# Kernel optimization log

Measured on AMD Instinct MI355X. Metric: run time of the kernel, lower is better.

## Reference

```python
import jax, jax.numpy as jnp
import numpy as np

IN_FEAT, H_FEAT, NUM_CLASSES = 7, 8, 2
N_NODES, N_EDGES, N_GRAPHS = 40000, 640000, 64
DIMS = [IN_FEAT, H_FEAT, H_FEAT * 2, H_FEAT * 4, H_FEAT * 8, H_FEAT * 16]  # 7,8,16,32,64,128


def setup_inputs() -> dict:
    key = jax.random.key(0)
    ks = jax.random.split(key, 20)
    inp = {
        "x": jax.random.normal(ks[0], (N_NODES, IN_FEAT), dtype=jnp.float32),
        "edge_index": jax.random.randint(ks[1], (2, N_EDGES), 0, N_NODES, dtype=jnp.int32),
        "edge_attr": jax.random.uniform(ks[2], (N_EDGES,), dtype=jnp.float32),
        "batch": jnp.sort(jax.random.randint(ks[3], (N_NODES,), 0, N_GRAPHS, dtype=jnp.int32)),
    }
    # GraphConv params: lin_rel (with bias) applied to aggregated messages,
    # lin_root (no bias) applied to x itself. Stored as [in, out]; y = x @ W.
    for i in range(5):
        fi, fo = DIMS[i], DIMS[i + 1]
        s = 1.0 / np.sqrt(fi)
        inp[f"w_rel{i+1}"] = jax.random.uniform(ks[4 + 3 * i], (fi, fo), minval=-s, maxval=s, dtype=jnp.float32)
        inp[f"b_rel{i+1}"] = jax.random.uniform(ks[5 + 3 * i], (fo,), minval=-s, maxval=s, dtype=jnp.float32)
        inp[f"w_root{i+1}"] = jax.random.uniform(ks[6 + 3 * i], (fi, fo), minval=-s, maxval=s, dtype=jnp.float32)
    s = 1.0 / np.sqrt(DIMS[-1])
    inp["w_lin"] = jax.random.uniform(ks[19], (DIMS[-1], NUM_CLASSES), minval=-s, maxval=s, dtype=jnp.float32)
    inp["b_lin"] = jax.random.uniform(jax.random.fold_in(key, 99), (NUM_CLASSES,), minval=-s, maxval=s, dtype=jnp.float32)
    return inp


def graph_conv(x, src, dst, ew, w_rel, b_rel, w_root):
    # message: edge_weight * x[src]; aggregate by sum at dst (PyG GraphConv, aggr='add')
    msg = x[src] * ew[:, None]                               # [E, Fin]
    agg = jax.ops.segment_sum(msg, dst, num_segments=N_NODES)  # [N, Fin]
    return agg @ w_rel + b_rel + x @ w_root                  # [N, Fout]


def reference(x, edge_index, edge_attr, batch,
              w_rel1, b_rel1, w_root1, w_rel2, b_rel2, w_root2,
              w_rel3, b_rel3, w_root3, w_rel4, b_rel4, w_root4,
              w_rel5, b_rel5, w_root5, w_lin, b_lin):
    src, dst = edge_index[0], edge_index[1]
    h = x
    params = [(w_rel1, b_rel1, w_root1), (w_rel2, b_rel2, w_root2),
              (w_rel3, b_rel3, w_root3), (w_rel4, b_rel4, w_root4),
              (w_rel5, b_rel5, w_root5)]
    for wr, br, wo in params:
        h = graph_conv(h, src, dst, edge_attr, wr, br, wo)
    pooled = jax.ops.segment_sum(h, batch, num_segments=N_GRAPHS)  # [G, 128]
    return pooled @ w_lin + b_lin                                  # [G, 2]
```

## Files before the change

### kernel.cpp

```cpp
#include <hip/hip_runtime.h>

#define N_NODES 40000
#define N_EDGES 640000
#define N_GRAPHS 64

typedef unsigned short u16;
typedef unsigned int u32;
typedef __attribute__((ext_vector_type(8))) short bf16x8;
typedef __attribute__((ext_vector_type(4))) float f32x4;

static inline int cdiv(long long a, int b) { return (int)((a + b - 1) / b); }

__device__ __forceinline__ u16 f2bf(float f) {
    u32 u = __float_as_uint(f);
    u32 r = (u + 0x7fffu + ((u >> 16) & 1u)) >> 16;
    return (u16)r;
}
__device__ __forceinline__ u32 packpair(float a, float b) {
    return (u32)f2bf(a) | ((u32)f2bf(b) << 16);
}
__device__ __forceinline__ void unpack8(uint4 q, float* o) {
    o[0] = __uint_as_float(q.x << 16); o[1] = __uint_as_float(q.x & 0xffff0000u);
    o[2] = __uint_as_float(q.y << 16); o[3] = __uint_as_float(q.y & 0xffff0000u);
    o[4] = __uint_as_float(q.z << 16); o[5] = __uint_as_float(q.z & 0xffff0000u);
    o[6] = __uint_as_float(q.w << 16); o[7] = __uint_as_float(q.w & 0xffff0000u);
}
__device__ __forceinline__ void fma4(float4& a, float s, const float4& w) {
    a.x = fmaf(s, w.x, a.x);
    a.y = fmaf(s, w.y, a.y);
    a.z = fmaf(s, w.z, a.z);
    a.w = fmaf(s, w.w, a.w);
}

__global__ __launch_bounds__(256) void hist_kernel(const int* __restrict__ dst,
                                                   int* __restrict__ deg) {
    int e = blockIdx.x * 256 + threadIdx.x;
    if (e < N_EDGES) atomicAdd(&deg[dst[e]], 1);
}

__global__ __launch_bounds__(1024) void scan_part(const int* __restrict__ deg,
                                                  int* __restrict__ row_start,
                                                  int* __restrict__ bsum) {
    __shared__ int wtot[16], woff[16];
    int tid = threadIdx.x;
    int i = blockIdx.x * 1024 + tid;
    int v = (i < N_NODES) ? deg[i] : 0;
    int lane = tid & 63, wid = tid >> 6;
    int inc = v;
    #pragma unroll
    for (int off = 1; off < 64; off <<= 1) {
        int y = __shfl_up(inc, off, 64);
        if (lane >= off) inc += y;
    }
    if (lane == 63) wtot[wid] = inc;
    __syncthreads();
    if (tid < 16) {
        int b = wtot[tid];
        #pragma unroll
        for (int off = 1; off < 16; off <<= 1) {
            int y = __shfl_up(b, off, 16);
            if ((tid & 15) >= off) b += y;
        }
        woff[tid] = b - wtot[tid];
        if (tid == 15) bsum[blockIdx.x] = b;
    }
    __syncthreads();
    if (i <= N_NODES) row_start[i] = woff[wid] + inc - v;
}

__global__ __launch_bounds__(1024) void scan_add(int* __restrict__ row_start,
                                                 const int* __restrict__ bsum,
                                                 int* __restrict__ cursor) {
    __shared__ int sbase;
    int tid = threadIdx.x;
    if (tid < 64) {
        int b = (tid < blockIdx.x) ? bsum[tid] : 0;
        #pragma unroll
        for (int off = 32; off; off >>= 1) b += __shfl_xor(b, off, 64);
        if (tid == 0) sbase = b;
    }
    __syncthreads();
    int i = blockIdx.x * 1024 + tid;
    if (i <= N_NODES) {
        int v = row_start[i] + sbase;
        row_start[i] = v;
        if (i < N_NODES) cursor[i] = v;
    }
}

__global__ __launch_bounds__(256) void scatter_kernel(const int* __restrict__ src,
                                                      const int* __restrict__ dst,
                                                      const float* __restrict__ ew,
                                                      int* __restrict__ cursor,
                                                      int2* __restrict__ csr_pair) {
    int e = blockIdx.x * 256 + threadIdx.x;
    if (e >= N_EDGES) return;
    int pos = atomicAdd(&cursor[dst[e]], 1);
    int2 q;
    q.x = src[e];
    q.y = __float_as_int(ew[e]);
    csr_pair[pos] = q;
}

__device__ __forceinline__ void pack_one(int idx, int K, int FOUT,
                                         const float* __restrict__ wrel,
                                         const float* __restrict__ wroot,
                                         u16* __restrict__ out) {
    int j = idx & 7;
    int lane = (idx >> 3) & 63;
    int ksnt = idx >> 9;
    int KS = K >> 5;
    int nt = ksnt / KS, ks = ksnt - nt * KS;
    int k = ks * 32 + (lane >> 4) * 8 + j;
    int col = nt * 16 + (lane & 15);
    float v = (k < K / 2) ? wrel[k * FOUT + col] : wroot[(k - K / 2) * FOUT + col];
    out[idx] = f2bf(v);
}

__global__ __launch_bounds__(256) void pack_weights(const float* __restrict__ wr3, const float* __restrict__ wo3,
                                                    const float* __restrict__ wr4, const float* __restrict__ wo4,
                                                    const float* __restrict__ wr5, const float* __restrict__ wo5,
                                                    u16* __restrict__ p3, u16* __restrict__ p4, u16* __restrict__ p5) {
    int tid = blockIdx.x * 256 + threadIdx.x;
    if (tid < 1024)        pack_one(tid,         32,  32,  wr3, wo3, p3);
    else if (tid < 5120)   pack_one(tid - 1024,  64,  64,  wr4, wo4, p4);
    else if (tid < 21504)  pack_one(tid - 5120, 128, 128,  wr5, wo5, p5);
}

template<int SLOG>
__global__ __launch_bounds__(256) void gather1(const float* __restrict__ x,
                                               const int* __restrict__ rs,
                                               const int2* __restrict__ pair,
                                               float* __restrict__ agg) {
    const int S = 1 << SLOG;
    long long tid = (long long)blockIdx.x * 256 + threadIdx.x;
    int n = (int)(tid >> (3 + SLOG));
    if (n >= N_NODES) return;
    int sub = (int)(tid & ((8 << SLOG) - 1));
    int f = sub & 7;
    int half = sub >> 3;
    int beg = rs[n], end = rs[n + 1];
    float acc = 0.f;
    int p = beg + half;
    int s = 0; float w = 0.f;
    if (p < end) { int2 q = pair[p]; s = q.x; w = __int_as_float(q.y); }
    while (p < end) {
        float v = (f < 7) ? x[(long long)s * 7 + f] : 0.f;
        float wc = w;
        int pn = p + S;
        if (pn < end) { int2 q = pair[pn]; s = q.x; w = __int_as_float(q.y); }
        acc = fmaf(wc, v, acc);
        p = pn;
    }
    #pragma unroll
    for (int d = 8; d < (8 << SLOG); d <<= 1) acc += __shfl_xor(acc, d, 64);
    if (half == 0 && f < 7) agg[(long long)n * 7 + f] = acc;
}

template<int LOGF, int SLOG, int IN_STRIDE, int IN_OFF, int OUT_STRIDE, int OUT_OFF>
__global__ __launch_bounds__(256) void gather_bf16(const u16* __restrict__ hbuf,
                                                   const int* __restrict__ rs,
                                                   const int2* __restrict__ pair,
                                                   u16* __restrict__ obuf) {
    const int S = 1 << SLOG;
    long long tid = (long long)blockIdx.x * 256 + threadIdx.x;
    int n = (int)(tid >> (LOGF + SLOG));
    if (n >= N_NODES) return;
    int sub = (int)(tid & ((1 << (LOGF + SLOG)) - 1));
    int c = sub & ((1 << LOGF) - 1);
    int half = sub >> LOGF;
    const u16* base = hbuf + IN_OFF + c * 8;
    int beg = rs[n], end = rs[n + 1];
    float acc[8] = {0.f, 0.f, 0.f, 0.f, 0.f, 0.f, 0.f, 0.f};
    int p = beg + half;
    int s = 0; float w = 0.f;
    if (p < end) { int2 q = pair[p]; s = q.x; w = __int_as_float(q.y); }
    while (p < end) {
        uint4 rq = *(const uint4*)(base + (long long)s * IN_STRIDE);
        float wc = w;
        int pn = p + S;
        if (pn < end) { int2 q = pair[pn]; s = q.x; w = __int_as_float(q.y); }
        float tv[8];
        unpack8(rq, tv);
        #pragma unroll
        for (int j = 0; j < 8; ++j) acc[j] = fmaf(wc, tv[j], acc[j]);
        p = pn;
    }
    #pragma unroll
    for (int d = (1 << LOGF); d < (1 << (LOGF + SLOG)); d <<= 1) {
        #pragma unroll
        for (int j = 0; j < 8; ++j) acc[j] += __shfl_xor(acc[j], d, 64);
    }
    if (half == 0) {
        uint4 o;
        o.x = packpair(acc[0], acc[1]); o.y = packpair(acc[2], acc[3]);
        o.z = packpair(acc[4], acc[5]); o.w = packpair(acc[6], acc[7]);
        *(uint4*)(obuf + (long long)n * OUT_STRIDE + OUT_OFF + c * 8) = o;
    }
}

__global__ __launch_bounds__(256) void node1(const float* __restrict__ agg,
                                             const float* __restrict__ x,
                                             const float* __restrict__ wr,
                                             const float* __restrict__ br,
                                             const float* __restrict__ wo,
                                             u16* __restrict__ obuf) {
    __shared__ float swr[56], swo[56], sb[8];
    if (threadIdx.x < 56) { swr[threadIdx.x] = wr[threadIdx.x]; swo[threadIdx.x] = wo[threadIdx.x]; }
    if (threadIdx.x < 8) sb[threadIdx.x] = br[threadIdx.x];
    __syncthreads();
    int n = blockIdx.x * 256 + threadIdx.x;
    if (n >= N_NODES) return;
    float a[7], h[7];
    #pragma unroll
    for (int i = 0; i < 7; ++i) {
        a[i] = agg[(long long)n * 7 + i];
        h[i] = x[(long long)n * 7 + i];
    }
    float o[8];
    #pragma unroll
    for (int j = 0; j < 8; ++j) {
        float s = sb[j];
        #pragma unroll
        for (int i = 0; i < 7; ++i) s = fmaf(a[i], swr[i * 8 + j], fmaf(h[i], swo[i * 8 + j], s));
        o[j] = s;
    }
    uint4 q;
    q.x = packpair(o[0], o[1]); q.y = packpair(o[2], o[3]);
    q.z = packpair(o[4], o[5]); q.w = packpair(o[6], o[7]);
    *(uint4*)(obuf + (long long)n * 16 + 8) = q;
}

template<int K, int FOUT, int FO_TILE, int NT, int OUT_STRIDE, int OUT_OFF>
__global__ __launch_bounds__(256) void node_mm(const u16* __restrict__ abuf,
                                               const float* __restrict__ w_rel,
                                               const float* __restrict__ b_rel,
                                               const float* __restrict__ w_root,
                                               u16* __restrict__ obuf) {
    constexpr int FG = FO_TILE / 4;
    constexpr int SLOTS = 256 / FG;
    constexpr int BN = SLOTS * NT;
    __shared__ float sw[K][FO_TILE];
    for (int i = threadIdx.x; i < K * FO_TILE; i += 256) {
        int k = i / FO_TILE, j = i % FO_TILE;
        sw[k][j] = (k < K / 2) ? w_rel[k * FOUT + j]
                               : w_root[(k - K / 2) * FOUT + j];
    }
    __syncthreads();
    int fg = threadIdx.x % FG;
    int slot = threadIdx.x / FG;
    int n0 = blockIdx.x * BN + slot * NT;
    float4 bias = *(const float4*)&b_rel[fg * 4];
    float4 acc[NT];
    #pragma unroll
    for (int t = 0; t < NT; ++t) acc[t] = bias;

    #pragma unroll
    for (int kc = 0; kc < K / 8; ++kc) {
        float4 wv[8];
        #pragma unroll
        for (int k = 0; k < 8; ++k) wv[k] = *(const float4*)&sw[kc * 8 + k][fg * 4];
        #pragma unroll
        for (int t = 0; t < NT; ++t) {
            int n = n0 + t;
            if (n < N_NODES) {
                uint4 q = *(const uint4*)(abuf + (long long)n * K + kc * 8);
                float av[8];
                unpack8(q, av);
                #pragma unroll
                for (int k = 0; k < 8; ++k) fma4(acc[t], av[k], wv[k]);
            }
        }
    }
    #pragma unroll
    for (int t = 0; t < NT; ++t) {
        int n = n0 + t;
        if (n < N_NODES) {
            uint2 o;
            o.x = packpair(acc[t].x, acc[t].y);
            o.y = packpair(acc[t].z, acc[t].w);
            *(uint2*)(obuf + (long long)n * OUT_STRIDE + OUT_OFF + fg * 4) = o;
        }
    }
}

template<int K, int FOUT, int OUT_STRIDE, int OUT_OFF, bool POOL>
__global__ __launch_bounds__(64) void node_mfma(const u16* __restrict__ abuf,
                                                const u16* __restrict__ bpack,
                                                const float* __restrict__ b_rel,
                                                u16* __restrict__ obuf,
                                                const int* __restrict__ batch,
                                                float* __restrict__ pooled) {
    constexpr int NT = FOUT / 16;
    constexpr int KS = K / 32;
    int lane = threadIdx.x;
    int tile = blockIdx.x;
    int col = lane & 15;
    int node_a = tile * 16 + col;
    int kgrp = (lane >> 4) * 8;

    f32x4 acc[NT];
    #pragma unroll
    for (int nt = 0; nt < NT; ++nt) {
        float bv = b_rel[nt * 16 + col];
        acc[nt] = (f32x4){bv, bv, bv, bv};
    }

    const u16* arow = abuf + (long long)node_a * K + kgrp;
    #pragma unroll
    for (int ks = 0; ks < KS; ++ks) {
        bf16x8 af = *(const bf16x8*)(arow + ks * 32);
        #pragma unroll
        for (int nt = 0; nt < NT; ++nt) {
            bf16x8 bf = *(const bf16x8*)(bpack + (((nt * KS + ks) << 6) + lane) * 8);
            acc[nt] = __builtin_amdgcn_mfma_f32_16x16x32_bf16(af, bf, acc[nt], 0, 0, 0);
        }
    }

    int row0 = tile * 16 + (lane >> 4) * 4;
    if constexpr (!POOL) {
        #pragma unroll
        for (int nt = 0; nt < NT; ++nt)
            #pragma unroll
            for (int r = 0; r < 4; ++r)
                obuf[(long long)(row0 + r) * OUT_STRIDE + OUT_OFF + nt * 16 + col] =
                    f2bf(acc[nt][r]);
    } else {
        int b_first = batch[tile * 16];
        int b_last = batch[tile * 16 + 15];
        if (b_first == b_last) {
            #pragma unroll
            for (int nt = 0; nt < NT; ++nt) {
                float s = acc[nt][0] + acc[nt][1] + acc[nt][2] + acc[nt][3];
                s += __shfl_xor(s, 16, 64);
                s += __shfl_xor(s, 32, 64);
                if (lane < 16) atomicAdd(&pooled[b_first * FOUT + nt * 16 + col], s);
            }
        } else {
            #pragma unroll
            for (int r = 0; r < 4; ++r) {
                int g = batch[row0 + r];
                #pragma unroll
                for (int nt = 0; nt < NT; ++nt)
                    atomicAdd(&pooled[g * FOUT + nt * 16 + col], acc[nt][r]);
            }
        }
    }
}

__global__ void final_kernel(const float* __restrict__ pooled,
                             const float* __restrict__ w_lin,
                             const float* __restrict__ b_lin,
                             float* __restrict__ out) {
    int tid = threadIdx.x;
    int g = tid >> 1;
    int c = tid & 1;
    float acc = b_lin[c];
    #pragma unroll 8
    for (int fi = 0; fi < 128; ++fi)
        acc += pooled[g * 128 + fi] * w_lin[fi * 2 + c];
    out[g * 2 + c] = acc;
}

extern "C" void kernel_launch(void* const* d_in, const int* in_sizes, int n_in,
                              void* d_out, int out_size, void* d_ws, size_t ws_size,
                              hipStream_t stream) {
    const float* x     = (const float*)d_in[0];
    const int*   ei    = (const int*)d_in[1];
    const float* ea    = (const float*)d_in[2];
    const int*   batch = (const int*)d_in[3];
    const int* src = ei;
    const int* dst = ei + N_EDGES;

    const float* w_rel[5], *b_rel[5], *w_root[5];
    for (int i = 0; i < 5; ++i) {
        w_rel[i]  = (const float*)d_in[4 + 3 * i];
        b_rel[i]  = (const float*)d_in[5 + 3 * i];
        w_root[i] = (const float*)d_in[6 + 3 * i];
    }
    const float* w_lin = (const float*)d_in[19];
    const float* b_lin = (const float*)d_in[20];
    float* out = (float*)d_out;

    float* agg1    = (float*)d_ws;
    u16*   buf2    = (u16*)(agg1 + 280000);
    u16*   buf3    = buf2 + 640000;
    u16*   buf4    = buf3 + 1280000;
    u16*   buf5    = buf4 + 2560000;
    float* pooled  = (float*)(buf5 + 5120000);
    u16*   p3      = (u16*)(pooled + N_GRAPHS * 128);
    u16*   p4      = p3 + 1024;
    u16*   p5      = p4 + 4096;
    int2*  csr_pair= (int2*)(p5 + 16384);
    int*   deg     = (int*)(csr_pair + N_EDGES);
    int*   rs      = deg + N_NODES;
    int*   cursor  = rs + N_NODES + 1;
    int*   bsum    = cursor + N_NODES;

    const int BLK = 256;
    const int EB = cdiv(N_EDGES, BLK);

    pack_weights<<<84, BLK, 0, stream>>>(w_rel[2], w_root[2], w_rel[3], w_root[3],
                                         w_rel[4], w_root[4], p3, p4, p5);
    hipMemsetAsync(deg, 0, (size_t)N_NODES * sizeof(int), stream);
    hist_kernel<<<EB, BLK, 0, stream>>>(dst, deg);
    scan_part<<<40, 1024, 0, stream>>>(deg, rs, bsum);
    scan_add<<<40, 1024, 0, stream>>>(rs, bsum, cursor);
    scatter_kernel<<<EB, BLK, 0, stream>>>(src, dst, ea, cursor, csr_pair);

    gather1<2><<<cdiv((long long)N_NODES * 32, BLK), BLK, 0, stream>>>(x, rs, csr_pair, agg1);
    node1<<<cdiv(N_NODES, 256), BLK, 0, stream>>>(agg1, x, w_rel[0], b_rel[0], w_root[0], buf2);

    gather_bf16<0, 3, 16, 8, 16, 0><<<cdiv((long long)N_NODES * 8, BLK), BLK, 0, stream>>>(
        buf2, rs, csr_pair, buf2);
    node_mm<16, 16, 16, 4, 32, 16><<<cdiv(N_NODES, 256), BLK, 0, stream>>>(
        buf2, w_rel[1], b_rel[1], w_root[1], buf3);

    gather_bf16<1, 3, 32, 16, 32, 0><<<cdiv((long long)N_NODES * 16, BLK), BLK, 0, stream>>>(
        buf3, rs, csr_pair, buf3);
    node_mfma<32, 32, 64, 32, false><<<2500, 64, 0, stream>>>(
        buf3, p3, b_rel[2], buf4, nullptr, nullptr);

    gather_bf16<2, 3, 64, 32, 64, 0><<<cdiv((long long)N_NODES * 32, BLK), BLK, 0, stream>>>(
        buf4, rs, csr_pair, buf4);
    node_mfma<64, 64, 128, 64, false><<<2500, 64, 0, stream>>>(
        buf4, p4, b_rel[3], buf5, nullptr, nullptr);

    gather_bf16<3, 3, 128, 64, 128, 0><<<cdiv((long long)N_NODES * 64, BLK), BLK, 0, stream>>>(
        buf5, rs, csr_pair, buf5);
    hipMemsetAsync(pooled, 0, (size_t)N_GRAPHS * 128 * sizeof(float), stream);
    node_mfma<128, 128, 0, 0, true><<<2500, 64, 0, stream>>>(
        buf5, p5, b_rel[4], nullptr, batch, pooled);

    final_kernel<<<1, 128, 0, stream>>>(pooled, w_lin, b_lin, out);
}
```

Baseline: 254.1 us.

## Fuse per-layer neighbor gather with MFMA node transform via LDS staging

Measured after the change: 275.7 us. 1.09x slower.

```diff
diff --git a/kernel.cpp b/kernel.cpp
--- a/kernel.cpp
+++ b/kernel.cpp
@@ -24,12 +24,6 @@
     o[2] = __uint_as_float(q.y << 16); o[3] = __uint_as_float(q.y & 0xffff0000u);
     o[4] = __uint_as_float(q.z << 16); o[5] = __uint_as_float(q.z & 0xffff0000u);
     o[6] = __uint_as_float(q.w << 16); o[7] = __uint_as_float(q.w & 0xffff0000u);
-}
-__device__ __forceinline__ void fma4(float4& a, float s, const float4& w) {
-    a.x = fmaf(s, w.x, a.x);
-    a.y = fmaf(s, w.y, a.y);
-    a.z = fmaf(s, w.z, a.z);
-    a.w = fmaf(s, w.w, a.w);
 }
 
 __global__ __launch_bounds__(256) void hist_kernel(const int* __restrict__ dst,
@@ -102,59 +96,48 @@
     csr_pair[pos] = q;
 }
 
-__device__ __forceinline__ void pack_one(int idx, int K, int FOUT,
+__device__ __forceinline__ void pack_one(int idx, int KS, int Kreal, int FOUT,
                                          const float* __restrict__ wrel,
                                          const float* __restrict__ wroot,
                                          u16* __restrict__ out) {
     int j = idx & 7;
     int lane = (idx >> 3) & 63;
-    int ksnt = idx >> 9;
-    int KS = K >> 5;
-    int nt = ksnt / KS, ks = ksnt - nt * KS;
+    int rest = idx >> 9;
+    int nt = rest / KS, ks = rest - nt * KS;
     int k = ks * 32 + (lane >> 4) * 8 + j;
     int col = nt * 16 + (lane & 15);
-    float v = (k < K / 2) ? wrel[k * FOUT + col] : wroot[(k - K / 2) * FOUT + col];
+    float v = 0.f;
+    if (k < Kreal / 2) v = wrel[k * FOUT + col];
+    else if (k < Kreal) v = wroot[(k - Kreal / 2) * FOUT + col];
     out[idx] = f2bf(v);
 }
 
-__global__ __launch_bounds__(256) void pack_weights(const float* __restrict__ wr3, const float* __restrict__ wo3,
-                                                    const float* __restrict__ wr4, const float* __restrict__ wo4,
-                                                    const float* __restrict__ wr5, const float* __restrict__ wo5,
-                                                    u16* __restrict__ p3, u16* __restrict__ p4, u16* __restrict__ p5) {
+__global__ __launch_bounds__(256) void pack_weights(
+        const float* __restrict__ wr2, const float* __restrict__ wo2,
+        const float* __restrict__ wr3, const float* __restrict__ wo3,
+        const float* __restrict__ wr4, const float* __restrict__ wo4,
+        const float* __restrict__ wr5, const float* __restrict__ wo5,
+        u16* __restrict__ p2, u16* __restrict__ p3,
+        u16* __restrict__ p4, u16* __restrict__ p5) {
     int tid = blockIdx.x * 256 + threadIdx.x;
-    if (tid < 1024)        pack_one(tid,         32,  32,  wr3, wo3, p3);
-    else if (tid < 5120)   pack_one(tid - 1024,  64,  64,  wr4, wo4, p4);
-    else if (tid < 21504)  pack_one(tid - 5120, 128, 128,  wr5, wo5, p5);
-}
-
-template<int SLOG>
-__global__ __launch_bounds__(256) void gather1(const float* __restrict__ x,
-                                               const int* __restrict__ rs,
-                                               const int2* __restrict__ pair,
-                                               float* __restrict__ agg) {
-    const int S = 1 << SLOG;
-    long long tid = (long long)blockIdx.x * 256 + threadIdx.x;
-    int n = (int)(tid >> (3 + SLOG));
+    if (tid < 512)         pack_one(tid,         1,  16,  16,  wr2, wo2, p2);
+    else if (tid < 1536)   pack_one(tid - 512,   1,  32,  32,  wr3, wo3, p3);
+    else if (tid < 5632)   pack_one(tid - 1536,  2,  64,  64,  wr4, wo4, p4);
+    else if (tid < 22016)  pack_one(tid - 5632,  4, 128, 128,  wr5, wo5, p5);
+}
+
+__global__ __launch_bounds__(256) void convert_x(const float* __restrict__ x,
+                                                 u16* __restrict__ xbf) {
+    int n = blockIdx.x * 256 + threadIdx.x;
     if (n >= N_NODES) return;
-    int sub = (int)(tid & ((8 << SLOG) - 1));
-    int f = sub & 7;
-    int half = sub >> 3;
-    int beg = rs[n], end = rs[n + 1];
-    float acc = 0.f;
-    int p = beg + half;
-    int s = 0; float w = 0.f;
-    if (p < end) { int2 q = pair[p]; s = q.x; w = __int_as_float(q.y); }
-    while (p < end) {
-        float v = (f < 7) ? x[(long long)s * 7 + f] : 0.f;
-        float wc = w;
-        int pn = p + S;
-        if (pn < end) { int2 q = pair[pn]; s = q.x; w = __int_as_float(q.y); }
-        acc = fmaf(wc, v, acc);
-        p = pn;
-    }
-    #pragma unroll
-    for (int d = 8; d < (8 << SLOG); d <<= 1) acc += __shfl_xor(acc, d, 64);
-    if (half == 0 && f < 7) agg[(long long)n * 7 + f] = acc;
+    float v[8];
+    #pragma unroll
+    for (int i = 0; i < 7; ++i) v[i] = x[n * 7 + i];
+    v[7] = 0.f;
+    uint4 q;
+    q.x = packpair(v[0], v[1]); q.y = packpair(v[2], v[3]);
+    q.z = packpair(v[4], v[5]); q.w = packpair(v[6], v[7]);
+    *(uint4*)(xbf + (long long)n * 8) = q;
 }
 
 template<int LOGF, int SLOG, int IN_STRIDE, int IN_OFF, int OUT_STRIDE, int OUT_OFF>
@@ -199,24 +182,23 @@
     }
 }
 
-__global__ __launch_bounds__(256) void node1(const float* __restrict__ agg,
-                                             const float* __restrict__ x,
-                                             const float* __restrict__ wr,
-                                             const float* __restrict__ br,
-                                             const float* __restrict__ wo,
-                                             u16* __restrict__ obuf) {
+__global__ __launch_bounds__(256) void node1b(const u16* __restrict__ agg1,
+                                              const u16* __restrict__ xbf,
+                                              const float* __restrict__ wr,
+                                              const float* __restrict__ br,
+                                              const float* __restrict__ wo,
+                                              u16* __restrict__ h2) {
     __shared__ float swr[56], swo[56], sb[8];
     if (threadIdx.x < 56) { swr[threadIdx.x] = wr[threadIdx.x]; swo[threadIdx.x] = wo[threadIdx.x]; }
     if (threadIdx.x < 8) sb[threadIdx.x] = br[threadIdx.x];
     __syncthreads();
     int n = blockIdx.x * 256 + threadIdx.x;
     if (n >= N_NODES) return;
-    float a[7], h[7];
-    #pragma unroll
-    for (int i = 0; i < 7; ++i) {
-        a[i] = agg[(long long)n * 7 + i];
-        h[i] = x[(long long)n * 7 + i];
-    }
+    float a[8], h[8];
+    uint4 qa = *(const uint4*)(agg1 + (long long)n * 8);
+    uint4 qh = *(const uint4*)(xbf + (long long)n * 8);
+    unpack8(qa, a);
+    unpack8(qh, h);
     float o[8];
     #pragma unroll
     for (int j = 0; j < 8; ++j) {
@@ -228,121 +210,136 @@
     uint4 q;
     q.x = packpair(o[0], o[1]); q.y = packpair(o[2], o[3]);
     q.z = packpair(o[4], o[5]); q.w = packpair(o[6], o[7]);
-    *(uint4*)(obuf + (long long)n * 16 + 8) = q;
-}
-
-template<int K, int FOUT, int FO_TILE, int NT, int OUT_STRIDE, int OUT_OFF>
-__global__ __launch_bounds__(256) void node_mm(const u16* __restrict__ abuf,
-                                               const float* __restrict__ w_rel,
-                                               const float* __restrict__ b_rel,
-                                               const float* __restrict__ w_root,
-                                               u16* __restrict__ obuf) {
-    constexpr int FG = FO_TILE / 4;
-    constexpr int SLOTS = 256 / FG;
-    constexpr int BN = SLOTS * NT;
-    __shared__ float sw[K][FO_TILE];
-    for (int i = threadIdx.x; i < K * FO_TILE; i += 256) {
-        int k = i / FO_TILE, j = i % FO_TILE;
-        sw[k][j] = (k < K / 2) ? w_rel[k * FOUT + j]
-                               : w_root[(k - K / 2) * FOUT + j];
+    *(uint4*)(h2 + (long long)n * 8) = q;
+}
+
+template<int LOGC, int FOUT, bool POOL>
+__global__ __launch_bounds__(256) void fused_layer(const u16* __restrict__ hin,
+                                                   const int* __restrict__ rs,
+                                                   const int2* __restrict__ pair,
+                                                   const u16* __restrict__ bpack,
+                                                   const float* __restrict__ b_rel,
+                                                   u16* __restrict__ hout,
+                                                   const int* __restrict__ batch,
+                                                   float* __restrict__ pooled) {
+    constexpr int FIN = 8 << LOGC;
+    constexpr int KREAL = 2 * FIN;
+    constexpr int K = (KREAL < 32) ? 32 : KREAL;
+    constexpr int KS = K / 32;
+    constexpr int NT = FOUT / 16;
+    constexpr int NTW = (NT + 3) / 4;
+    constexpr int LDK = K + 8;
+    constexpr int CHUNKS = 1 << LOGC;
+    constexpr int SPLIT = 64 >> LOGC;
+
+    __shared__ u16 lds[16][LDK];
+
+    int tid = threadIdx.x;
+    int wave = tid >> 6;
+    int lane = tid & 63;
+    int node0 = blockIdx.x * 16;
+
+    if constexpr (KREAL < K) {
+        for (int i = tid; i < 16 * (K - KREAL); i += 256) {
+            int r = i / (K - KREAL), cc = i % (K - KREAL);
+            lds[r][KREAL + cc] = 0;
+        }
+    }
+    {
+        constexpr int CH = FIN / 8;
+        for (int i = tid; i < 16 * CH; i += 256) {
+            int r = i / CH, cc = i % CH;
+            uint4 v = *(const uint4*)(hin + (long long)(node0 + r) * FIN + cc * 8);
+            *(uint4*)&lds[r][FIN + cc * 8] = v;
+        }
+    }
+
+    int c = lane & (CHUNKS - 1);
+    int half = lane >> LOGC;
+    #pragma unroll
+    for (int rnd = 0; rnd < 4; ++rnd) {
+        int nl = rnd * 4 + wave;
+        int n = node0 + nl;
+        int beg = rs[n], end = rs[n + 1];
+        float acc[8] = {0.f, 0.f, 0.f, 0.f, 0.f, 0.f, 0.f, 0.f};
+        int p = beg + half;
+        int s = 0; float w = 0.f;
+        if (p < end) { int2 q = pair[p]; s = q.x; w = __int_as_float(q.y); }
+        while (p < end) {
+            uint4 rq = *(const uint4*)(hin + (long long)s * FIN + c * 8);
+            float wc = w;
+            int pn = p + SPLIT;
+            if (pn < end) { int2 q = pair[pn]; s = q.x; w = __int_as_float(q.y); }
+            float tv[8];
+            unpack8(rq, tv);
+            #pragma unroll
+            for (int j = 0; j < 8; ++j) acc[j] = fmaf(wc, tv[j], acc[j]);
+            p = pn;
+        }
+        #pragma unroll
+        for (int d = CHUNKS; d < 64; d <<= 1) {
+            #pragma unroll
+            for (int j = 0; j < 8; ++j) acc[j] += __shfl_xor(acc[j], d, 64);
+        }
+        if (half == 0) {
+            uint4 o;
+            o.x = packpair(acc[0], acc[1]); o.y = packpair(acc[2], acc[3]);
+            o.z = packpair(acc[4], acc[5]); o.w = packpair(acc[6], acc[7]);
+            *(uint4*)&lds[nl][c * 8] = o;
+        }
     }
     __syncthreads();
-    int fg = threadIdx.x % FG;
-    int slot = threadIdx.x / FG;
-    int n0 = blockIdx.x * BN + slot * NT;
-    float4 bias = *(const float4*)&b_rel[fg * 4];
-    float4 acc[NT];
-    #pragma unroll
-    for (int t = 0; t < NT; ++t) acc[t] = bias;
-
-    #pragma unroll
-    for (int kc = 0; kc < K / 8; ++kc) {
-        float4 wv[8];
-        #pragma unroll
-        for (int k = 0; k < 8; ++k) wv[k] = *(const float4*)&sw[kc * 8 + k][fg * 4];
-        #pragma unroll
-        for (int t = 0; t < NT; ++t) {
-            int n = n0 + t;
-            if (n < N_NODES) {
-                uint4 q = *(const uint4*)(abuf + (long long)n * K + kc * 8);
-                float av[8];
-                unpack8(q, av);
-                #pragma unroll
-                for (int k = 0; k < 8; ++k) fma4(acc[t], av[k], wv[k]);
-            }
-        }
-    }
-    #pragma unroll
-    for (int t = 0; t < NT; ++t) {
-        int n = n0 + t;
-        if (n < N_NODES) {
-            uint2 o;
-            o.x = packpair(acc[t].x, acc[t].y);
-            o.y = packpair(acc[t].z, acc[t].w);
-            *(uint2*)(obuf + (long long)n * OUT_STRIDE + OUT_OFF + fg * 4) = o;
-        }
-    }
-}
-
-template<int K, int FOUT, int OUT_STRIDE, int OUT_OFF, bool POOL>
-__global__ __launch_bounds__(64) void node_mfma(const u16* __restrict__ abuf,
-                                                const u16* __restrict__ bpack,
-                                                const float* __restrict__ b_rel,
-                                                u16* __restrict__ obuf,
-                                                const int* __restrict__ batch,
-                                                float* __restrict__ pooled) {
-    constexpr int NT = FOUT / 16;
-    constexpr int KS = K / 32;
-    int lane = threadIdx.x;
-    int tile = blockIdx.x;
-    int col = lane & 15;
-    int node_a = tile * 16 + col;
-    int kgrp = (lane >> 4) * 8;
-
-    f32x4 acc[NT];
-    #pragma unroll
-    for (int nt = 0; nt < NT; ++nt) {
-        float bv = b_rel[nt * 16 + col];
-        acc[nt] = (f32x4){bv, bv, bv, bv};
-    }
-
-    const u16* arow = abuf + (long long)node_a * K + kgrp;
+
+    int ntbase = wave * NTW;
+    if (ntbase >= NT) return;
+
+    int colc = lane & 15;
+    int kg = (lane >> 4) * 8;
+
+    f32x4 acc[NTW];
+    #pragma unroll
+    for (int t = 0; t < NTW; ++t) {
+        float bv = b_rel[(ntbase + t) * 16 + colc];
+        acc[t] = (f32x4){bv, bv, bv, bv};
+    }
+
     #pragma unroll
     for (int ks = 0; ks < KS; ++ks) {
-        bf16x8 af = *(const bf16x8*)(arow + ks * 32);
-        #pragma unroll
-        for (int nt = 0; nt < NT; ++nt) {
-            bf16x8 bf = *(const bf16x8*)(bpack + (((nt * KS + ks) << 6) + lane) * 8);
-            acc[nt] = __builtin_amdgcn_mfma_f32_16x16x32_bf16(af, bf, acc[nt], 0, 0, 0);
-        }
-    }
-
-    int row0 = tile * 16 + (lane >> 4) * 4;
+        bf16x8 af = *(const bf16x8*)&lds[colc][kg + ks * 32];
+        #pragma unroll
+        for (int t = 0; t < NTW; ++t) {
+            int ntg = ntbase + t;
+            bf16x8 bf = *(const bf16x8*)(bpack + (((ntg * KS + ks) << 6) + lane) * 8);
+            acc[t] = __builtin_amdgcn_mfma_f32_16x16x32_bf16(af, bf, acc[t], 0, 0, 0);
+        }
+    }
+
+    int row0 = (lane >> 4) * 4;
     if constexpr (!POOL) {
         #pragma unroll
-        for (int nt = 0; nt < NT; ++nt)
+        for (int t = 0; t < NTW; ++t)
             #pragma unroll
             for (int r = 0; r < 4; ++r)
-                obuf[(long long)(row0 + r) * OUT_STRIDE + OUT_OFF + nt * 16 + col] =
-                    f2bf(acc[nt][r]);
+                hout[(long long)(node0 + row0 + r) * FOUT + (ntbase + t) * 16 + colc] =
+                    f2bf(acc[t][r]);
     } else {
-        int b_first = batch[tile * 16];
-        int b_last = batch[tile * 16 + 15];
+        int b_first = batch[node0];
+        int b_last = batch[node0 + 15];
         if (b_first == b_last) {
             #pragma unroll
-            for (int nt = 0; nt < NT; ++nt) {
-                float s = acc[nt][0] + acc[nt][1] + acc[nt][2] + acc[nt][3];
-                s += __shfl_xor(s, 16, 64);
-                s += __shfl_xor(s, 32, 64);
-                if (lane < 16) atomicAdd(&pooled[b_first * FOUT + nt * 16 + col], s);
+            for (int t = 0; t < NTW; ++t) {
+                float s2 = acc[t][0] + acc[t][1] + acc[t][2] + acc[t][3];
+                s2 += __shfl_xor(s2, 16, 64);
+                s2 += __shfl_xor(s2, 32, 64);
+                if (lane < 16) atomicAdd(&pooled[b_first * FOUT + (ntbase + t) * 16 + colc], s2);
             }
         } else {
             #pragma unroll
             for (int r = 0; r < 4; ++r) {
-                int g = batch[row0 + r];
+                int g = batch[node0 + row0 + r];
                 #pragma unroll
-                for (int nt = 0; nt < NT; ++nt)
-                    atomicAdd(&pooled[g * FOUT + nt * 16 + col], acc[nt][r]);
+                for (int t = 0; t < NTW; ++t)
+                    atomicAdd(&pooled[g * FOUT + (ntbase + t) * 16 + colc], acc[t][r]);
             }
         }
     }
@@ -382,13 +379,15 @@
     const float* b_lin = (const float*)d_in[20];
     float* out = (float*)d_out;
 
-    float* agg1    = (float*)d_ws;
-    u16*   buf2    = (u16*)(agg1 + 280000);
-    u16*   buf3    = buf2 + 640000;
-    u16*   buf4    = buf3 + 1280000;
-    u16*   buf5    = buf4 + 2560000;
-    float* pooled  = (float*)(buf5 + 5120000);
-    u16*   p3      = (u16*)(pooled + N_GRAPHS * 128);
+    u16*   xbf     = (u16*)d_ws;
+    u16*   agg1    = xbf + 320000;
+    u16*   h2      = agg1 + 320000;
+    u16*   h3      = h2 + 320000;
+    u16*   h4      = h3 + 640000;
+    u16*   h5      = h4 + 1280000;
+    float* pooled  = (float*)(h5 + 2560000);
+    u16*   p2      = (u16*)(pooled + N_GRAPHS * 128);
+    u16*   p3      = p2 + 512;
     u16*   p4      = p3 + 1024;
     u16*   p5      = p4 + 4096;
     int2*  csr_pair= (int2*)(p5 + 16384);
@@ -400,37 +399,25 @@
     const int BLK = 256;
     const int EB = cdiv(N_EDGES, BLK);
 
-    pack_weights<<<84, BLK, 0, stream>>>(w_rel[2], w_root[2], w_rel[3], w_root[3],
-                                         w_rel[4], w_root[4], p3, p4, p5);
+    convert_x<<<cdiv(N_NODES, BLK), BLK, 0, stream>>>(x, xbf);
+    pack_weights<<<86, BLK, 0, stream>>>(w_rel[1], w_root[1], w_rel[2], w_root[2],
+                                         w_rel[3], w_root[3], w_rel[4], w_root[4],
+                                         p2, p3, p4, p5);
     hipMemsetAsync(deg, 0, (size_t)N_NODES * sizeof(int), stream);
+    hipMemsetAsync(pooled, 0, (size_t)N_GRAPHS * 128 * sizeof(float), stream);
     hist_kernel<<<EB, BLK, 0, stream>>>(dst, deg);
     scan_part<<<40, 1024, 0, stream>>>(deg, rs, bsum);
     scan_add<<<40, 1024, 0, stream>>>(rs, bsum, cursor);
     scatter_kernel<<<EB, BLK, 0, stream>>>(src, dst, ea, cursor, csr_pair);
 
-    gather1<2><<<cdiv((long long)N_NODES * 32, BLK), BLK, 0, stream>>>(x, rs, csr_pair, agg1);
-    node1<<<cdiv(N_NODES, 256), BLK, 0, stream>>>(agg1, x, w_rel[0], b_rel[0], w_root[0], buf2);
-
-    gather_bf16<0, 3, 16, 8, 16, 0><<<cdiv((long long)N_NODES * 8, BLK), BLK, 0, stream>>>(
-        buf2, rs, csr_pair, buf2);
-    node_mm<16, 16, 16, 4, 32, 16><<<cdiv(N_NODES, 256), BLK, 0, stream>>>(
-        buf2, w_rel[1], b_rel[1], w_root[1], buf3);
-
-    gather_bf16<1, 3, 32, 16, 32, 0><<<cdiv((long long)N_NODES * 16, BLK), BLK, 0, stream>>>(
-        buf3, rs, csr_pair, buf3);
-    node_mfma<32, 32, 64, 32, false><<<2500, 64, 0, stream>>>(
-        buf3, p3, b_rel[2], buf4, nullptr, nullptr);
-
-    gather_bf16<2, 3, 64, 32, 64, 0><<<cdiv((long long)N_NODES * 32, BLK), BLK, 0, stream>>>(
-        buf4, rs, csr_pair, buf4);
-    node_mfma<64, 64, 128, 64, false><<<2500, 64, 0, stream>>>(
-        buf4, p4, b_rel[3], buf5, nullptr, nullptr);
-
-    gather_bf16<3, 3, 128, 64, 128, 0><<<cdiv((long long)N_NODES * 64, BLK), BLK, 0, stream>>>(
-        buf5, rs, csr_pair, buf5);
-    hipMemsetAsync(pooled, 0, (size_t)N_GRAPHS * 128 * sizeof(float), stream);
-    node_mfma<128, 128, 0, 0, true><<<2500, 64, 0, stream>>>(
-        buf5, p5, b_rel[4], nullptr, batch, pooled);
+    gather_bf16<0, 3, 8, 0, 8, 0><<<cdiv((long long)N_NODES * 8, BLK), BLK, 0, stream>>>(
+        xbf, rs, csr_pair, agg1);
+    node1b<<<cdiv(N_NODES, BLK), BLK, 0, stream>>>(agg1, xbf, w_rel[0], b_rel[0], w_root[0], h2);
+
+    fused_layer<0, 16, false><<<2500, BLK, 0, stream>>>(h2, rs, csr_pair, p2, b_rel[1], h3, nullptr, nullptr);
+    fused_layer<1, 32, false><<<2500, BLK, 0, stream>>>(h3, rs, csr_pair, p3, b_rel[2], h4, nullptr, nullptr);
+    fused_layer<2, 64, false><<<2500, BLK, 0, stream>>>(h4, rs, csr_pair, p4, b_rel[3], h5, nullptr, nullptr);
+    fused_layer<3, 128, true><<<2500, BLK, 0, stream>>>(h5, rs, csr_pair, p5, b_rel[4], nullptr, batch, pooled);
 
     final_kernel<<<1, 128, 0, stream>>>(pooled, w_lin, b_lin, out);
 }
```
